# Performance work log

Hardware: AMD Instinct MI355X
Metric: run time of the kernel (lower is better)

## Reference

```python
import jax, jax.numpy as jnp
import numpy as np

LOG_CLAMP = -100.0  # torch F.binary_cross_entropy clamps log terms at -100


def setup_inputs() -> dict:
    key = jax.random.key(0)
    k1, k2, k3 = jax.random.split(key, 3)
    B, N, M, K = 8, 2048, 2048, 1000000
    pred_perm = jax.random.uniform(k1, (B, N, M), dtype=jnp.float32)
    gt_perm = jax.random.uniform(k2, (B, N, M), dtype=jnp.float32)
    all_matches = jax.random.randint(k3, (K, 2), 0, N, dtype=jnp.int64 if jax.config.jax_enable_x64 else jnp.int32)
    return {"pred_perm": pred_perm, "gt_perm": gt_perm, "all_matches": all_matches}


def reference(pred_perm, gt_perm, all_matches):
    # Gather matched entries: [B, K]
    rows = all_matches[:, 0]
    cols = all_matches[:, 1]
    p = pred_perm[:, rows, cols].astype(jnp.float32)
    g = gt_perm[:, rows, cols].astype(jnp.float32)
    log_p = jnp.maximum(jnp.log(p), LOG_CLAMP)
    log_1mp = jnp.maximum(jnp.log1p(-p), LOG_CLAMP)
    bce = -(g * log_p + (1.0 - g) * log_1mp)  # per-element BCE (scalar reduction='mean' on scalars == identity)
    # Original sums over batch and matches, divides only by num matches
    return jnp.sum(bce) / all_matches.shape[0]
```

## Files before the change

kernel.cpp:

```cpp
#include <hip/hip_runtime.h>


static constexpr int       N_ROWS      = 2048;
static constexpr int       M_DIM       = 2048;
static constexpr long long PLANE       = 2048LL * 2048LL;
static constexpr int       B_DIM       = 8;
static constexpr float     LOG_CLAMP_F = -100.0f;

__global__ __launch_bounds__(256) void count_kernel(
    const int2* __restrict__ matches, unsigned* __restrict__ cnt, int K)
{
    const int stride = gridDim.x * blockDim.x;
    for (int k = blockIdx.x * blockDim.x + threadIdx.x; k < K; k += stride) {
        const int2 rc = matches[k];
        atomicAdd(&cnt[rc.x * M_DIM + rc.y], 1u);
    }
}

__global__ __launch_bounds__(256) void bce_sweep_kernel(
    const float*    __restrict__ pred,
    const float*    __restrict__ gt,
    const unsigned* __restrict__ cnt,
    float*          __restrict__ out,
    float inv_k)
{
    float acc = 0.0f;
    const long long nChunks = PLANE / 4;
    const long long stride  = (long long)gridDim.x * blockDim.x;

    for (long long c = (long long)blockIdx.x * blockDim.x + threadIdx.x;
         c < nChunks; c += stride) {
        const long long e = c * 4;
        const uint4 cc = *reinterpret_cast<const uint4*>(&cnt[e]);
        const float w0 = (float)cc.x, w1 = (float)cc.y,
                    w2 = (float)cc.z, w3 = (float)cc.w;

        #pragma unroll
        for (int b = 0; b < B_DIM; ++b) {
            const float4 p4 = *reinterpret_cast<const float4*>(&pred[b * PLANE + e]);
            const float4 g4 = *reinterpret_cast<const float4*>(&gt  [b * PLANE + e]);

            const float p[4] = {p4.x, p4.y, p4.z, p4.w};
            const float g[4] = {g4.x, g4.y, g4.z, g4.w};
            const float w[4] = {w0, w1, w2, w3};
            #pragma unroll
            for (int i = 0; i < 4; ++i) {
                const float lp  = fmaxf(logf(p[i]),    LOG_CLAMP_F);
                const float l1m = fmaxf(log1pf(-p[i]), LOG_CLAMP_F);
                acc -= w[i] * (g[i] * lp + (1.0f - g[i]) * l1m);
            }
        }
    }

    #pragma unroll
    for (int off = 32; off > 0; off >>= 1)
        acc += __shfl_down(acc, off, 64);
    __shared__ float wsum[4];
    const int lane = threadIdx.x & 63;
    const int wid  = threadIdx.x >> 6;
    if (lane == 0) wsum[wid] = acc;
    __syncthreads();
    if (threadIdx.x == 0)
        atomicAdd(out, (wsum[0] + wsum[1] + wsum[2] + wsum[3]) * inv_k);
}

__global__ __launch_bounds__(256) void bce_gather_kernel(
    const float* __restrict__ pred,
    const float* __restrict__ gt,
    const int2*  __restrict__ matches,
    float*       __restrict__ out,
    int K, float inv_k)
{
    float acc = 0.0f;
    const int stride = gridDim.x * blockDim.x;
    for (int k = blockIdx.x * blockDim.x + threadIdx.x; k < K; k += stride) {
        const int2 rc = matches[k];
        const long long base = (long long)rc.x * M_DIM + rc.y;
        float p[B_DIM], g[B_DIM];
        #pragma unroll
        for (int b = 0; b < B_DIM; ++b) {
            p[b] = pred[base + b * PLANE];
            g[b] = gt[base + b * PLANE];
        }
        #pragma unroll
        for (int b = 0; b < B_DIM; ++b) {
            const float lp  = fmaxf(logf(p[b]),    LOG_CLAMP_F);
            const float l1m = fmaxf(log1pf(-p[b]), LOG_CLAMP_F);
            acc -= g[b] * lp + (1.0f - g[b]) * l1m;
        }
    }
    #pragma unroll
    for (int off = 32; off > 0; off >>= 1)
        acc += __shfl_down(acc, off, 64);
    __shared__ float wsum[4];
    const int lane = threadIdx.x & 63;
    const int wid  = threadIdx.x >> 6;
    if (lane == 0) wsum[wid] = acc;
    __syncthreads();
    if (threadIdx.x == 0)
        atomicAdd(out, (wsum[0] + wsum[1] + wsum[2] + wsum[3]) * inv_k);
}

extern "C" void kernel_launch(void* const* d_in, const int* in_sizes, int n_in,
                              void* d_out, int out_size, void* d_ws, size_t ws_size,
                              hipStream_t stream) {
    const float* pred    = (const float*)d_in[0];
    const float* gt      = (const float*)d_in[1];
    const int2*  matches = (const int2*)d_in[2];
    const int K = in_sizes[2] / 2;

    hipMemsetAsync(d_out, 0, sizeof(float), stream);

    const size_t need_counts = (size_t)PLANE * sizeof(unsigned);

    if (ws_size >= need_counts) {
        unsigned* cnt = (unsigned*)d_ws;
        hipMemsetAsync(cnt, 0, need_counts, stream);
        count_kernel<<<2048, 256, 0, stream>>>(matches, cnt, K);
        bce_sweep_kernel<<<2048, 256, 0, stream>>>(
            pred, gt, cnt, (float*)d_out, 1.0f / (float)K);
    } else {
        bce_gather_kernel<<<4096, 256, 0, stream>>>(
            pred, gt, matches, (float*)d_out, K, 1.0f / (float)K);
    }
}
```

Measured before the change: 347.5 us.

## Precompute per-position batch-summed BCE then gather-sum over matches

Replaces the atomic histogram of match counts plus the weighted sweep with two kernels. The first computes the batch-summed BCE for every (row,col) position into a workspace plane. The second gathers that plane at each match and reduces, with four loads in flight per thread. This drops the count memset and the atomic histogram at the cost of writing and then randomly reading a 16 MB plane. It also switches logf/log1pf to fast __log2f scaled by ln2, which may lose accuracy for p near 0 or 1.

```diff
diff --git a/kernel.cpp b/kernel.cpp
--- a/kernel.cpp
+++ b/kernel.cpp
@@ -1,56 +1,66 @@
 #include <hip/hip_runtime.h>
 
 
-static constexpr int       N_ROWS      = 2048;
 static constexpr int       M_DIM       = 2048;
 static constexpr long long PLANE       = 2048LL * 2048LL;
 static constexpr int       B_DIM       = 8;
 static constexpr float     LOG_CLAMP_F = -100.0f;
+static constexpr float     LN2F        = 0.69314718055994530942f;
 
-__global__ __launch_bounds__(256) void count_kernel(
-    const int2* __restrict__ matches, unsigned* __restrict__ cnt, int K)
-{
-    const int stride = gridDim.x * blockDim.x;
-    for (int k = blockIdx.x * blockDim.x + threadIdx.x; k < K; k += stride) {
-        const int2 rc = matches[k];
-        atomicAdd(&cnt[rc.x * M_DIM + rc.y], 1u);
-    }
+__device__ __forceinline__ float bce_term(float p, float g) {
+    const float lp  = fmaxf(__log2f(p)        * LN2F, LOG_CLAMP_F);
+    const float l1m = fmaxf(__log2f(1.0f - p) * LN2F, LOG_CLAMP_F);
+    return -(g * (lp - l1m) + l1m);
 }
 
-__global__ __launch_bounds__(256) void bce_sweep_kernel(
-    const float*    __restrict__ pred,
-    const float*    __restrict__ gt,
-    const unsigned* __restrict__ cnt,
-    float*          __restrict__ out,
-    float inv_k)
+__global__ __launch_bounds__(256) void bce_precompute_kernel(
+    const float* __restrict__ pred,
+    const float* __restrict__ gt,
+    float*       __restrict__ S)
 {
-    float acc = 0.0f;
     const long long nChunks = PLANE / 4;
     const long long stride  = (long long)gridDim.x * blockDim.x;
 
     for (long long c = (long long)blockIdx.x * blockDim.x + threadIdx.x;
          c < nChunks; c += stride) {
         const long long e = c * 4;
-        const uint4 cc = *reinterpret_cast<const uint4*>(&cnt[e]);
-        const float w0 = (float)cc.x, w1 = (float)cc.y,
-                    w2 = (float)cc.z, w3 = (float)cc.w;
-
+        float s0 = 0.f, s1 = 0.f, s2 = 0.f, s3 = 0.f;
         #pragma unroll
         for (int b = 0; b < B_DIM; ++b) {
             const float4 p4 = *reinterpret_cast<const float4*>(&pred[b * PLANE + e]);
             const float4 g4 = *reinterpret_cast<const float4*>(&gt  [b * PLANE + e]);
+            s0 += bce_term(p4.x, g4.x);
+            s1 += bce_term(p4.y, g4.y);
+            s2 += bce_term(p4.z, g4.z);
+            s3 += bce_term(p4.w, g4.w);
+        }
+        *reinterpret_cast<float4*>(&S[e]) = make_float4(s0, s1, s2, s3);
+    }
+}
 
-            const float p[4] = {p4.x, p4.y, p4.z, p4.w};
-            const float g[4] = {g4.x, g4.y, g4.z, g4.w};
-            const float w[4] = {w0, w1, w2, w3};
-            #pragma unroll
-            for (int i = 0; i < 4; ++i) {
-                const float lp  = fmaxf(logf(p[i]),    LOG_CLAMP_F);
-                const float l1m = fmaxf(log1pf(-p[i]), LOG_CLAMP_F);
-                acc -= w[i] * (g[i] * lp + (1.0f - g[i]) * l1m);
-            }
-        }
+__global__ __launch_bounds__(256) void gather_sum_kernel(
+    const float* __restrict__ S,
+    const int2*  __restrict__ matches,
+    float*       __restrict__ out,
+    int K, float inv_k)
+{
+    float acc = 0.0f;
+    const int T = gridDim.x * blockDim.x;
+    int k = blockIdx.x * blockDim.x + threadIdx.x;
+
+    for (; k + 3 * T < K; k += 4 * T) {
+        const int2 a = matches[k];
+        const int2 b = matches[k + T];
+        const int2 c = matches[k + 2 * T];
+        const int2 d = matches[k + 3 * T];
+        const float va = S[(long long)a.x * M_DIM + a.y];
+        const float vb = S[(long long)b.x * M_DIM + b.y];
+        const float vc = S[(long long)c.x * M_DIM + c.y];
+        const float vd = S[(long long)d.x * M_DIM + d.y];
+        acc += (va + vb) + (vc + vd);
     }
+    for (; k < K; k += T)
+        acc += S[(long long)matches[k].x * M_DIM + matches[k].y];
 
     #pragma unroll
     for (int off = 32; off > 0; off >>= 1)
@@ -83,11 +93,8 @@
             g[b] = gt[base + b * PLANE];
         }
         #pragma unroll
-        for (int b = 0; b < B_DIM; ++b) {
-            const float lp  = fmaxf(logf(p[b]),    LOG_CLAMP_F);
-            const float l1m = fmaxf(log1pf(-p[b]), LOG_CLAMP_F);
-            acc -= g[b] * lp + (1.0f - g[b]) * l1m;
-        }
+        for (int b = 0; b < B_DIM; ++b)
+            acc += bce_term(p[b], g[b]);
     }
     #pragma unroll
     for (int off = 32; off > 0; off >>= 1)
@@ -111,14 +118,13 @@
 
     hipMemsetAsync(d_out, 0, sizeof(float), stream);
 
-    const size_t need_counts = (size_t)PLANE * sizeof(unsigned);
+    const size_t need = (size_t)PLANE * sizeof(float);
 
-    if (ws_size >= need_counts) {
-        unsigned* cnt = (unsigned*)d_ws;
-        hipMemsetAsync(cnt, 0, need_counts, stream);
-        count_kernel<<<2048, 256, 0, stream>>>(matches, cnt, K);
-        bce_sweep_kernel<<<2048, 256, 0, stream>>>(
-            pred, gt, cnt, (float*)d_out, 1.0f / (float)K);
+    if (ws_size >= need) {
+        float* S = (float*)d_ws;
+        bce_precompute_kernel<<<2048, 256, 0, stream>>>(pred, gt, S);
+        gather_sum_kernel   <<<1024, 256, 0, stream>>>(
+            S, matches, (float*)d_out, K, 1.0f / (float)K);
     } else {
         bce_gather_kernel<<<4096, 256, 0, stream>>>(
             pred, gt, matches, (float*)d_out, K, 1.0f / (float)K);
```

Measured after the change: 309.1 us. 11.0% less time.
